# Optimization experiments

Hardware: AMD Instinct MI355X
Metric: run time of the kernel (lower is better)

Reference implementation:

```python
import jax, jax.numpy as jnp
import numpy as np

B, S, D = 1, 4096, 1024
H, W = 16, 512            # heads, window_size
HD = D // H               # head_dim = 64


def setup_inputs() -> dict:
    key = jax.random.key(0)
    k1, k2, k3 = jax.random.split(key, 3)
    x = jax.random.normal(k1, (B, S, D), dtype=jnp.float32)
    w_qkv = jax.random.normal(k2, (D, 3 * D), dtype=jnp.float32) * 0.02
    w_out = jax.random.normal(k3, (D, D), dtype=jnp.float32) * 0.02
    return {"x": x, "w_qkv": w_qkv, "w_out": w_out}


def reference(x, w_qkv, w_out):
    b, s, d = x.shape
    qkv = x @ w_qkv                                   # [B,S,3D]
    q, k, v = jnp.split(qkv, 3, axis=-1)
    to_heads = lambda t: t.reshape(b, s, H, HD).transpose(0, 2, 1, 3)  # [B,H,S,hd]
    q, k, v = map(to_heads, (q, k, v))

    C = s // W                                        # number of chunks
    qc = q.reshape(b, H, C, W, HD)                    # [B,H,C,W,hd]
    kc = k.reshape(b, H, C, W, HD)
    vc = v.reshape(b, H, C, W, HD)

    # each chunk attends to [previous chunk, current chunk] of K/V (2W keys)
    zero = jnp.zeros_like(kc[:, :, :1])
    k_prev = jnp.concatenate([zero, kc[:, :, :-1]], axis=2)
    v_prev = jnp.concatenate([jnp.zeros_like(vc[:, :, :1]), vc[:, :, :-1]], axis=2)
    kcat = jnp.concatenate([k_prev, kc], axis=3)      # [B,H,C,2W,hd]
    vcat = jnp.concatenate([v_prev, vc], axis=3)

    scores = jnp.einsum('bhcqd,bhckd->bhcqk', qc, kcat) / (HD ** 0.5)

    # mask: causal (abs q_pos >= abs k_pos) and k_pos >= 0 (first chunk has no prev)
    wq = jnp.arange(W)
    jk = jnp.arange(2 * W)
    ci = jnp.arange(C)
    causal = (wq[:, None] + W) >= jk[None, :]                    # [W,2W]
    valid = (ci[:, None, None] * W + jk[None, None, :] - W) >= 0  # [C,1,2W]
    mask = causal[None] & valid                                   # [C,W,2W]

    scores = jnp.where(mask[None, None], scores, -jnp.inf)
    attn = jax.nn.softmax(scores, axis=-1)
    out = jnp.einsum('bhcqk,bhckd->bhcqd', attn, vcat)            # [B,H,C,W,hd]
    out = out.reshape(b, H, s, HD).transpose(0, 2, 1, 3).reshape(b, s, d)
    return out @ w_out
```

## Files before the change

### kernel.cpp

```cpp
#include <hip/hip_runtime.h>

typedef __attribute__((ext_vector_type(8))) short short8;
typedef __attribute__((ext_vector_type(4))) float f32x4;
typedef unsigned short u16;

__device__ __forceinline__ u16 f2bf(float f) {
  unsigned int u = __float_as_uint(f);
  u += 0x7fffu + ((u >> 16) & 1u);
  return (u16)(u >> 16);
}

__device__ __forceinline__ void gld16(const void* g, void* l) {
  __builtin_amdgcn_global_load_lds((const __attribute__((address_space(1))) void*)g,
                                   (__attribute__((address_space(3))) void*)l, 16, 0, 0);
}

__global__ __launch_bounds__(256) void cast_f32_to_bf16(const float* __restrict__ in,
                                                        u16* __restrict__ out, int n8) {
  int i = blockIdx.x * 256 + threadIdx.x;
  if (i >= n8) return;
  const f32x4* p = (const f32x4*)in;
  f32x4 a = p[i * 2];
  f32x4 b = p[i * 2 + 1];
  short8 o;
#pragma unroll
  for (int j = 0; j < 4; ++j) o[j] = (short)f2bf(a[j]);
#pragma unroll
  for (int j = 0; j < 4; ++j) o[4 + j] = (short)f2bf(b[j]);
  ((short8*)out)[i] = o;
}

__global__ __launch_bounds__(256) void transpose_cast(const float* __restrict__ w,
                                                      u16* __restrict__ wT, int K, int N) {
  __shared__ float tile[32][33];
  int n0 = blockIdx.x * 32, k0 = blockIdx.y * 32;
  int r = threadIdx.x >> 5;
  int c = threadIdx.x & 31;
#pragma unroll
  for (int i = 0; i < 4; ++i)
    tile[r + i * 8][c] = w[(size_t)(k0 + r + i * 8) * N + n0 + c];
  __syncthreads();
#pragma unroll
  for (int i = 0; i < 4; ++i)
    wT[(size_t)(n0 + r + i * 8) * K + k0 + c] = f2bf(tile[c][r + i * 8]);
}

__global__ __launch_bounds__(256) void transpose_v(const u16* __restrict__ vh,
                                                   u16* __restrict__ vt) {
  __shared__ u16 tile[32][33];
  const int s0 = blockIdx.x * 32, d0 = blockIdx.y * 32, h = blockIdx.z;
  const long hb = (long)h * 4096 * 64;
  const long hb2 = (long)h * 64 * 4096;
  const int r = threadIdx.x >> 5, c = threadIdx.x & 31;
#pragma unroll
  for (int i = 0; i < 4; ++i)
    tile[r + i * 8][c] = vh[hb + (long)(s0 + r + i * 8) * 64 + d0 + c];
  __syncthreads();
#pragma unroll
  for (int i = 0; i < 4; ++i)
    vt[hb2 + (long)(d0 + r + i * 8) * 4096 + s0 + c] = tile[c][r + i * 8];
}

template <int MODE, int BN>
__global__ __launch_bounds__(256) void gemm_bf16(
    const u16* __restrict__ A, const u16* __restrict__ Bt, float* __restrict__ C,
    u16* __restrict__ q_out, u16* __restrict__ k_out, u16* __restrict__ v_out,
    int M, int N, int K) {
  __shared__ __align__(16) u16 As[128][64];
  __shared__ __align__(16) u16 Bs[BN][64];
  constexpr int NW = BN / 32;
  const int t = threadIdx.x;
  const int lane = t & 63;
  const int wid = t >> 6;
  const int wm = wid >> 1, wn = wid & 1;
  const int l15 = lane & 15, lhi = lane >> 4;

  const int nbx = gridDim.x;
  const int bid = blockIdx.y * nbx + blockIdx.x;
  const int cpx = (nbx * gridDim.y) >> 3;
  const int wg = (bid & 7) * cpx + (bid >> 3);
  const int m0 = (wg / nbx) * 128;
  const int n0 = (wg % nbx) * BN;

  const int srow = lane >> 3;
  const int scol = ((lane & 7) ^ (lane >> 3)) * 8;

  f32x4 acc[4][NW];
#pragma unroll
  for (int mi = 0; mi < 4; ++mi)
#pragma unroll
    for (int ni = 0; ni < NW; ++ni) acc[mi][ni] = (f32x4){0.f, 0.f, 0.f, 0.f};

  for (int k0 = 0; k0 < K; k0 += 64) {
    __syncthreads();
#pragma unroll
    for (int i = 0; i < 4; ++i) {
      int cch = wid * 4 + i;
      int row = cch * 8 + srow;
      const u16* src = (MODE == 2)
          ? &A[((size_t)(k0 >> 6) * 4096 + m0 + row) * 64 + scol]
          : &A[(size_t)(m0 + row) * K + k0 + scol];
      gld16(src, &As[cch * 8][0]);
    }
#pragma unroll
    for (int i = 0; i < NW; ++i) {
      int cch = wid * NW + i;
      int row = cch * 8 + srow;
      gld16(&Bt[(size_t)(n0 + row) * K + k0 + scol], &Bs[cch * 8][0]);
    }
    __syncthreads();
#pragma unroll
    for (int kc = 0; kc < 2; ++kc) {
      short8 af[4], bf[NW];
#pragma unroll
      for (int mi = 0; mi < 4; ++mi) {
        int row = wm * 64 + mi * 16 + l15;
        af[mi] = *(const short8*)&As[row][((kc * 4 + lhi) ^ (l15 & 7)) * 8];
      }
#pragma unroll
      for (int ni = 0; ni < NW; ++ni) {
        int row = wn * (BN / 2) + ni * 16 + l15;
        bf[ni] = *(const short8*)&Bs[row][((kc * 4 + lhi) ^ (l15 & 7)) * 8];
      }
#pragma unroll
      for (int mi = 0; mi < 4; ++mi)
#pragma unroll
        for (int ni = 0; ni < NW; ++ni)
          acc[mi][ni] = __builtin_amdgcn_mfma_f32_16x16x32_bf16(af[mi], bf[ni], acc[mi][ni], 0, 0, 0);
    }
  }

  const float SCQ = 0.18033688011112042f;
#pragma unroll
  for (int mi = 0; mi < 4; ++mi)
#pragma unroll
    for (int ni = 0; ni < NW; ++ni)
#pragma unroll
      for (int r = 0; r < 4; ++r) {
        int row = m0 + wm * 64 + mi * 16 + lhi * 4 + r;
        int col = n0 + wn * (BN / 2) + ni * 16 + l15;
        float val = acc[mi][ni][r];
        if constexpr (MODE == 1) {
          int which = col >> 10;
          int d = col & 1023;
          int hh = d >> 6, hd = d & 63;
          if (which == 0)      q_out[((size_t)hh * 4096 + row) * 64 + hd] = f2bf(val * SCQ);
          else if (which == 1) k_out[((size_t)hh * 4096 + row) * 64 + hd] = f2bf(val);
          else                 v_out[((size_t)hh * 4096 + row) * 64 + hd] = f2bf(val);
        } else {
          C[(size_t)row * N + col] = val;
        }
      }
}

__global__ __launch_bounds__(256) void attn_kernel(
    const u16* __restrict__ qh,
    const u16* __restrict__ kh,
    const u16* __restrict__ vt,
    u16* __restrict__ outh) {
  __shared__ __align__(16) u16 Ks[2][64][64];
  __shared__ __align__(16) u16 Vt[2][65][64];
  __shared__ __align__(16) u16 Pl[4][32][72];

  const int t = threadIdx.x;
  const int lane = t & 63;
  const int w = t >> 6;
  const int l15 = lane & 15;
  const int lhi = lane >> 4;

  const int bid = blockIdx.x;
  const int wk = (bid & 7) * 64 + (bid >> 3);
  const int qt = wk & 3, c = (wk >> 2) & 7, h = wk >> 5;

  const long head_base = (long)h * 4096 * 64;
  const int q0 = qt * 128;
  const long q_gbase = head_base + (long)(c * 512 + q0) * 64;

  short8 qf[2][2];
#pragma unroll
  for (int mi = 0; mi < 2; ++mi)
#pragma unroll
    for (int kc = 0; kc < 2; ++kc)
      qf[mi][kc] = *(const short8*)&qh[q_gbase + (long)(w * 32 + mi * 16 + l15) * 64 + kc * 32 + lhi * 8];

  if (t < 128) Vt[t >> 6][64][t & 63] = 0x3F80;

  float m_run[8];
  f32x4 acc_o[2][4], acc_l[2];
#pragma unroll
  for (int i = 0; i < 8; ++i) m_run[i] = -1e30f;
#pragma unroll
  for (int mi = 0; mi < 2; ++mi) {
    acc_l[mi] = (f32x4){0.f, 0.f, 0.f, 0.f};
#pragma unroll
    for (int ni = 0; ni < 4; ++ni) acc_o[mi][ni] = (f32x4){0.f, 0.f, 0.f, 0.f};
  }

  const int kt_start = (c == 0) ? 8 : 0;
  const int kt_end = 2 * qt + 9;
  const long kv_base = head_base + ((long)c - 1) * 512 * 64;
  const long vt_hb = (long)h * 64 * 4096 + ((long)c - 1) * 512;

  const int srow = lane >> 3;
  const int sunit8 = ((lane & 7) ^ (lane >> 3)) * 8;

  {
    const int j0 = kt_start * 64;
#pragma unroll
    for (int i = 0; i < 2; ++i) {
      int cch = w * 2 + i;
      gld16(&kh[kv_base + (long)(j0 + cch * 8 + srow) * 64 + sunit8], &Ks[0][cch * 8][0]);
      gld16(&vt[vt_hb + (long)(cch * 8 + srow) * 4096 + j0 + sunit8], &Vt[0][cch * 8][0]);
    }
  }
  __syncthreads();

  int cur = 0;
  for (int kt = kt_start; kt <= kt_end; ++kt) {
    const int j0 = kt * 64;
    const int nxt = cur ^ 1;

    if (kt < kt_end) {
      const int j0n = j0 + 64;
#pragma unroll
      for (int i = 0; i < 2; ++i) {
        int cch = w * 2 + i;
        gld16(&kh[kv_base + (long)(j0n + cch * 8 + srow) * 64 + sunit8], &Ks[nxt][cch * 8][0]);
        gld16(&vt[vt_hb + (long)(cch * 8 + srow) * 4096 + j0n + sunit8], &Vt[nxt][cch * 8][0]);
      }
    }

    const bool active = (j0 <= q0 + w * 32 + 31 + 512);
    if (active) {
      f32x4 sa[2][4];
#pragma unroll
      for (int mi = 0; mi < 2; ++mi)
#pragma unroll
        for (int ni = 0; ni < 4; ++ni) sa[mi][ni] = (f32x4){0.f, 0.f, 0.f, 0.f};
#pragma unroll
      for (int kc = 0; kc < 2; ++kc) {
        short8 kf[4];
#pragma unroll
        for (int ni = 0; ni < 4; ++ni) {
          int row = ni * 16 + l15;
          kf[ni] = *(const short8*)&Ks[cur][row][((kc * 4 + lhi) ^ (l15 & 7)) * 8];
        }
#pragma unroll
        for (int mi = 0; mi < 2; ++mi)
#pragma unroll
          for (int ni = 0; ni < 4; ++ni)
            sa[mi][ni] = __builtin_amdgcn_mfma_f32_16x16x32_bf16(qf[mi][kc], kf[ni], sa[mi][ni], 0, 0, 0);
      }

      const int qrow0 = q0 + w * 32 + lhi * 4;
      const bool need_mask = (j0 + 63 > q0 + w * 32 + 512);
      float tmax[8];
#pragma unroll
      for (int i = 0; i < 8; ++i) tmax[i] = -1e30f;
      if (need_mask) {
#pragma unroll
        for (int mi = 0; mi < 2; ++mi)
#pragma unroll
          for (int ni = 0; ni < 4; ++ni) {
            int jj = j0 + ni * 16 + l15;
#pragma unroll
            for (int r = 0; r < 4; ++r) {
              float sv = sa[mi][ni][r];
              sv = (qrow0 + mi * 16 + r + 512 >= jj) ? sv : -1e30f;
              sa[mi][ni][r] = sv;
              tmax[mi * 4 + r] = fmaxf(tmax[mi * 4 + r], sv);
            }
          }
      } else {
#pragma unroll
        for (int mi = 0; mi < 2; ++mi)
#pragma unroll
          for (int ni = 0; ni < 4; ++ni)
#pragma unroll
            for (int r = 0; r < 4; ++r)
              tmax[mi * 4 + r] = fmaxf(tmax[mi * 4 + r], sa[mi][ni][r]);
      }
#pragma unroll
      for (int i = 0; i < 8; ++i)
#pragma unroll
        for (int d = 1; d < 16; d <<= 1)
          tmax[i] = fmaxf(tmax[i], __shfl_xor(tmax[i], d, 64));

      float corr[8];
#pragma unroll
      for (int i = 0; i < 8; ++i) {
        float mn = fmaxf(m_run[i], tmax[i]);
        corr[i] = __builtin_amdgcn_exp2f(m_run[i] - mn);
        m_run[i] = mn;
      }
#pragma unroll
      for (int mi = 0; mi < 2; ++mi)
#pragma unroll
        for (int ni = 0; ni < 4; ++ni)
#pragma unroll
          for (int r = 0; r < 4; ++r) {
            float p = __builtin_amdgcn_exp2f(sa[mi][ni][r] - m_run[mi * 4 + r]);
            Pl[w][mi * 16 + lhi * 4 + r][ni * 16 + l15] = f2bf(p);
          }
#pragma unroll
      for (int mi = 0; mi < 2; ++mi) {
#pragma unroll
        for (int r = 0; r < 4; ++r) acc_l[mi][r] *= corr[mi * 4 + r];
#pragma unroll
        for (int ni = 0; ni < 4; ++ni)
#pragma unroll
          for (int r = 0; r < 4; ++r) acc_o[mi][ni][r] *= corr[mi * 4 + r];
      }

#pragma unroll
      for (int k2 = 0; k2 < 2; ++k2) {
        short8 pf[2];
#pragma unroll
        for (int mi = 0; mi < 2; ++mi)
          pf[mi] = *(const short8*)&Pl[w][mi * 16 + l15][k2 * 32 + lhi * 8];
        short8 vones = *(const short8*)&Vt[cur][64][k2 * 32 + lhi * 8];
#pragma unroll
        for (int mi = 0; mi < 2; ++mi)
          acc_l[mi] = __builtin_amdgcn_mfma_f32_16x16x32_bf16(pf[mi], vones, acc_l[mi], 0, 0, 0);
#pragma unroll
        for (int ni = 0; ni < 4; ++ni) {
          int row = ni * 16 + l15;
          short8 vf = *(const short8*)&Vt[cur][row][((k2 * 4 + lhi) ^ (l15 & 7)) * 8];
#pragma unroll
          for (int mi = 0; mi < 2; ++mi)
            acc_o[mi][ni] = __builtin_amdgcn_mfma_f32_16x16x32_bf16(pf[mi], vf, acc_o[mi][ni], 0, 0, 0);
        }
      }
    }
    __syncthreads();
    cur = nxt;
  }

#pragma unroll
  for (int mi = 0; mi < 2; ++mi)
#pragma unroll
    for (int ni = 0; ni < 4; ++ni)
#pragma unroll
      for (int r = 0; r < 4; ++r) {
        int qq = q0 + w * 32 + mi * 16 + lhi * 4 + r;
        long s = (long)c * 512 + qq;
        float o = acc_o[mi][ni][r] / acc_l[mi][r];
        outh[(head_base + s * 64) + ni * 16 + l15] = f2bf(o);
      }
}

extern "C" void kernel_launch(void* const* d_in, const int* in_sizes, int n_in,
                              void* d_out, int out_size, void* d_ws, size_t ws_size,
                              hipStream_t stream) {
  const float* x = (const float*)d_in[0];
  const float* w_qkv = (const float*)d_in[1];
  const float* w_out = (const float*)d_in[2];
  float* out = (float*)d_out;

  u16* xb = (u16*)d_ws;
  u16* wqkvT = xb + 4096 * 1024;
  u16* woutT = wqkvT + 3072 * 1024;
  u16* qh = woutT + 1024 * 1024;
  u16* kh = qh + 16 * 4096 * 64;
  u16* vh = kh + 16 * 4096 * 64;
  u16* vt = xb;

  cast_f32_to_bf16<<<2048, 256, 0, stream>>>(x, xb, 4096 * 1024 / 8);
  transpose_cast<<<dim3(96, 32), 256, 0, stream>>>(w_qkv, wqkvT, 1024, 3072);
  transpose_cast<<<dim3(32, 32), 256, 0, stream>>>(w_out, woutT, 1024, 1024);

  gemm_bf16<1, 128><<<dim3(24, 32), 256, 0, stream>>>(xb, wqkvT, nullptr, qh, kh, vh,
                                                      4096, 3072, 1024);
  transpose_v<<<dim3(128, 2, 16), 256, 0, stream>>>(vh, vt);
  attn_kernel<<<512, 256, 0, stream>>>(qh, kh, vt, qh);
  gemm_bf16<2, 64><<<dim3(16, 32), 256, 0, stream>>>(qh, woutT, out, nullptr, nullptr, nullptr,
                                                     4096, 1024, 1024);
}
```

Baseline: 187.4 us.

## Transpose attention MFMAs so each lane owns one query row

Swaps the MFMA operand order in both QK^T and PV, so each lane holds a whole query row's scores across registers. Row max and row sum are then mostly in-register reductions with only two cross-lane shuffles, replacing the per-row 16-lane shuffle trees. The row sum is computed directly, so the extra ones-row MFMA in V^T is removed. P is stored as packed bf16 pairs in a padded uint LDS array, and the output is written with 4-wide vector stores. This adds more register pressure for the per-row arrays and relies on the new P layout staying free of bank conflicts.

Result: faster. 182.5 us (-2.6%).

```diff
diff --git a/kernel.cpp b/kernel.cpp
--- a/kernel.cpp
+++ b/kernel.cpp
@@ -2,6 +2,7 @@
 
 typedef __attribute__((ext_vector_type(8))) short short8;
 typedef __attribute__((ext_vector_type(4))) float f32x4;
+typedef __attribute__((ext_vector_type(4))) unsigned short us4;
 typedef unsigned short u16;
 
 __device__ __forceinline__ u16 f2bf(float f) {
@@ -159,8 +160,8 @@
     const u16* __restrict__ vt,
     u16* __restrict__ outh) {
   __shared__ __align__(16) u16 Ks[2][64][64];
-  __shared__ __align__(16) u16 Vt[2][65][64];
-  __shared__ __align__(16) u16 Pl[4][32][72];
+  __shared__ __align__(16) u16 Vt[2][64][64];
+  __shared__ __align__(16) unsigned int Pl[4][32][37];
 
   const int t = threadIdx.x;
   const int lane = t & 63;
@@ -183,18 +184,12 @@
     for (int kc = 0; kc < 2; ++kc)
       qf[mi][kc] = *(const short8*)&qh[q_gbase + (long)(w * 32 + mi * 16 + l15) * 64 + kc * 32 + lhi * 8];
 
-  if (t < 128) Vt[t >> 6][64][t & 63] = 0x3F80;
-
-  float m_run[8];
-  f32x4 acc_o[2][4], acc_l[2];
-#pragma unroll
-  for (int i = 0; i < 8; ++i) m_run[i] = -1e30f;
-#pragma unroll
-  for (int mi = 0; mi < 2; ++mi) {
-    acc_l[mi] = (f32x4){0.f, 0.f, 0.f, 0.f};
-#pragma unroll
-    for (int ni = 0; ni < 4; ++ni) acc_o[mi][ni] = (f32x4){0.f, 0.f, 0.f, 0.f};
-  }
+  float m_run[2] = {-1e30f, -1e30f}, l_run[2] = {0.f, 0.f};
+  f32x4 acc_o[2][4];
+#pragma unroll
+  for (int mi = 0; mi < 2; ++mi)
+#pragma unroll
+    for (int nd = 0; nd < 4; ++nd) acc_o[mi][nd] = (f32x4){0.f, 0.f, 0.f, 0.f};
 
   const int kt_start = (c == 0) ? 8 : 0;
   const int kt_end = 2 * qt + 9;
@@ -249,86 +244,75 @@
         for (int mi = 0; mi < 2; ++mi)
 #pragma unroll
           for (int ni = 0; ni < 4; ++ni)
-            sa[mi][ni] = __builtin_amdgcn_mfma_f32_16x16x32_bf16(qf[mi][kc], kf[ni], sa[mi][ni], 0, 0, 0);
-      }
-
-      const int qrow0 = q0 + w * 32 + lhi * 4;
+            sa[mi][ni] = __builtin_amdgcn_mfma_f32_16x16x32_bf16(kf[ni], qf[mi][kc], sa[mi][ni], 0, 0, 0);
+      }
+
       const bool need_mask = (j0 + 63 > q0 + w * 32 + 512);
-      float tmax[8];
-#pragma unroll
-      for (int i = 0; i < 8; ++i) tmax[i] = -1e30f;
-      if (need_mask) {
+#pragma unroll
+      for (int mi = 0; mi < 2; ++mi) {
+        const int qloc = q0 + w * 32 + mi * 16 + l15;
+        if (need_mask) {
+          const int lim = qloc + 512 - j0 - 4 * lhi;
+#pragma unroll
+          for (int ni = 0; ni < 4; ++ni)
+#pragma unroll
+            for (int r = 0; r < 4; ++r)
+              if (16 * ni + r > lim) sa[mi][ni][r] = -1e30f;
+        }
+        float v[16];
+#pragma unroll
+        for (int ni = 0; ni < 4; ++ni)
+#pragma unroll
+          for (int r = 0; r < 4; ++r) v[ni * 4 + r] = sa[mi][ni][r];
+#pragma unroll
+        for (int s = 8; s >= 1; s >>= 1)
+#pragma unroll
+          for (int k = 0; k < s; ++k) v[k] = fmaxf(v[k], v[k + s]);
+        float tm = v[0];
+        tm = fmaxf(tm, __shfl_xor(tm, 16, 64));
+        tm = fmaxf(tm, __shfl_xor(tm, 32, 64));
+
+        float mn = fmaxf(m_run[mi], tm);
+        float corr = __builtin_amdgcn_exp2f(m_run[mi] - mn);
+        m_run[mi] = mn;
+
+        float ps[16];
+#pragma unroll
+        for (int ni = 0; ni < 4; ++ni) {
+#pragma unroll
+          for (int r = 0; r < 4; ++r) ps[ni * 4 + r] = __builtin_amdgcn_exp2f(sa[mi][ni][r] - mn);
+          unsigned int p01 = (unsigned int)f2bf(ps[ni * 4 + 0]) | ((unsigned int)f2bf(ps[ni * 4 + 1]) << 16);
+          unsigned int p23 = (unsigned int)f2bf(ps[ni * 4 + 2]) | ((unsigned int)f2bf(ps[ni * 4 + 3]) << 16);
+          Pl[w][mi * 16 + l15][8 * ni + 2 * lhi + 0] = p01;
+          Pl[w][mi * 16 + l15][8 * ni + 2 * lhi + 1] = p23;
+        }
+#pragma unroll
+        for (int s = 8; s >= 1; s >>= 1)
+#pragma unroll
+          for (int k = 0; k < s; ++k) ps[k] += ps[k + s];
+        float ls = ps[0];
+        ls += __shfl_xor(ls, 16, 64);
+        ls += __shfl_xor(ls, 32, 64);
+        l_run[mi] = l_run[mi] * corr + ls;
+#pragma unroll
+        for (int nd = 0; nd < 4; ++nd)
+#pragma unroll
+          for (int r = 0; r < 4; ++r) acc_o[mi][nd][r] *= corr;
+      }
+
+#pragma unroll
+      for (int kc = 0; kc < 2; ++kc) {
+        short8 pf[2];
 #pragma unroll
         for (int mi = 0; mi < 2; ++mi)
-#pragma unroll
-          for (int ni = 0; ni < 4; ++ni) {
-            int jj = j0 + ni * 16 + l15;
-#pragma unroll
-            for (int r = 0; r < 4; ++r) {
-              float sv = sa[mi][ni][r];
-              sv = (qrow0 + mi * 16 + r + 512 >= jj) ? sv : -1e30f;
-              sa[mi][ni][r] = sv;
-              tmax[mi * 4 + r] = fmaxf(tmax[mi * 4 + r], sv);
-            }
-          }
-      } else {
-#pragma unroll
-        for (int mi = 0; mi < 2; ++mi)
-#pragma unroll
-          for (int ni = 0; ni < 4; ++ni)
-#pragma unroll
-            for (int r = 0; r < 4; ++r)
-              tmax[mi * 4 + r] = fmaxf(tmax[mi * 4 + r], sa[mi][ni][r]);
-      }
-#pragma unroll
-      for (int i = 0; i < 8; ++i)
-#pragma unroll
-        for (int d = 1; d < 16; d <<= 1)
-          tmax[i] = fmaxf(tmax[i], __shfl_xor(tmax[i], d, 64));
-
-      float corr[8];
-#pragma unroll
-      for (int i = 0; i < 8; ++i) {
-        float mn = fmaxf(m_run[i], tmax[i]);
-        corr[i] = __builtin_amdgcn_exp2f(m_run[i] - mn);
-        m_run[i] = mn;
-      }
-#pragma unroll
-      for (int mi = 0; mi < 2; ++mi)
-#pragma unroll
-        for (int ni = 0; ni < 4; ++ni)
-#pragma unroll
-          for (int r = 0; r < 4; ++r) {
-            float p = __builtin_amdgcn_exp2f(sa[mi][ni][r] - m_run[mi * 4 + r]);
-            Pl[w][mi * 16 + lhi * 4 + r][ni * 16 + l15] = f2bf(p);
-          }
-#pragma unroll
-      for (int mi = 0; mi < 2; ++mi) {
-#pragma unroll
-        for (int r = 0; r < 4; ++r) acc_l[mi][r] *= corr[mi * 4 + r];
-#pragma unroll
-        for (int ni = 0; ni < 4; ++ni)
-#pragma unroll
-          for (int r = 0; r < 4; ++r) acc_o[mi][ni][r] *= corr[mi * 4 + r];
-      }
-
-#pragma unroll
-      for (int k2 = 0; k2 < 2; ++k2) {
-        short8 pf[2];
-#pragma unroll
-        for (int mi = 0; mi < 2; ++mi)
-          pf[mi] = *(const short8*)&Pl[w][mi * 16 + l15][k2 * 32 + lhi * 8];
-        short8 vones = *(const short8*)&Vt[cur][64][k2 * 32 + lhi * 8];
-#pragma unroll
-        for (int mi = 0; mi < 2; ++mi)
-          acc_l[mi] = __builtin_amdgcn_mfma_f32_16x16x32_bf16(pf[mi], vones, acc_l[mi], 0, 0, 0);
-#pragma unroll
-        for (int ni = 0; ni < 4; ++ni) {
-          int row = ni * 16 + l15;
-          short8 vf = *(const short8*)&Vt[cur][row][((k2 * 4 + lhi) ^ (l15 & 7)) * 8];
+          pf[mi] = *(const short8*)&Pl[w][mi * 16 + l15][kc * 16 + lhi * 4];
+#pragma unroll
+        for (int nd = 0; nd < 4; ++nd) {
+          int row = nd * 16 + l15;
+          short8 vf = *(const short8*)&Vt[cur][row][((kc * 4 + lhi) ^ (l15 & 7)) * 8];
 #pragma unroll
           for (int mi = 0; mi < 2; ++mi)
-            acc_o[mi][ni] = __builtin_amdgcn_mfma_f32_16x16x32_bf16(pf[mi], vf, acc_o[mi][ni], 0, 0, 0);
+            acc_o[mi][nd] = __builtin_amdgcn_mfma_f32_16x16x32_bf16(vf, pf[mi], acc_o[mi][nd], 0, 0, 0);
         }
       }
     }
@@ -337,16 +321,17 @@
   }
 
 #pragma unroll
-  for (int mi = 0; mi < 2; ++mi)
-#pragma unroll
-    for (int ni = 0; ni < 4; ++ni)
-#pragma unroll
-      for (int r = 0; r < 4; ++r) {
-        int qq = q0 + w * 32 + mi * 16 + lhi * 4 + r;
-        long s = (long)c * 512 + qq;
-        float o = acc_o[mi][ni][r] / acc_l[mi][r];
-        outh[(head_base + s * 64) + ni * 16 + l15] = f2bf(o);
-      }
+  for (int mi = 0; mi < 2; ++mi) {
+    float inv = 1.f / l_run[mi];
+    long s = (long)c * 512 + q0 + w * 32 + mi * 16 + l15;
+#pragma unroll
+    for (int nd = 0; nd < 4; ++nd) {
+      us4 o;
+#pragma unroll
+      for (int r = 0; r < 4; ++r) o[r] = f2bf(acc_o[mi][nd][r] * inv);
+      *(us4*)&outh[head_base + s * 64 + nd * 16 + lhi * 4] = o;
+    }
+  }
 }
 
 extern "C" void kernel_launch(void* const* d_in, const int* in_sizes, int n_in,
```
